# Kernel tuning notes

Hardware: AMD Instinct MI355X
Metric: run time of the kernel (lower is better)

## Reference

```python
import jax, jax.numpy as jnp
import numpy as np

T, NA, ND, E, H, L = 4, 20000, 20000, 100000, 128, 2


def setup_inputs() -> dict:
    key = jax.random.key(0)
    ks = jax.random.split(key, 16)
    f = lambda k, s: jax.random.normal(k, s, dtype=jnp.float32)
    s = 0.05  # weight init scale
    inp = {
        "x_a": f(ks[0], (T, NA, H)),
        "x_d": f(ks[1], (T, ND, H)),
        "ea_ad": f(ks[2], (T, E, H)),
        "ea_da": f(ks[3], (T, E, H)),
        # edge_index rows: [src, dst]
        "ei_ad": jax.random.randint(ks[4], (T, 2, E), 0, NA, dtype=jnp.int32),
        "ei_da": jax.random.randint(ks[5], (T, 2, E), 0, ND, dtype=jnp.int32),
    }
    i = 6
    for et in ("ad", "da"):
        inp[f"w1_{et}"] = f(ks[i], (T, L, H, H)) * s; i += 1
        inp[f"b1_{et}"] = jnp.zeros((T, L, H), jnp.float32)
        inp[f"w2_{et}"] = f(ks[i], (T, L, H, H)) * s; i += 1
        inp[f"b2_{et}"] = jnp.zeros((T, L, H), jnp.float32)
        inp[f"eps_{et}"] = jnp.zeros((T, L), jnp.float32)
    return inp


def _gine(x_src, x_dst, ei, ea, w1, b1, w2, b2, eps, n_dst):
    # GINEConv: MLP((1+eps)*x_dst + sum_j relu(x_src[j] + edge_attr))
    msg = jax.nn.relu(x_src[ei[0]] + ea)                      # (E, H)
    agg = jax.ops.segment_sum(msg, ei[1], num_segments=n_dst)  # (n_dst, H)
    h = (1.0 + eps) * x_dst + agg
    return jax.nn.relu(h @ w1 + b1) @ w2 + b2


def _one_timestep(xa, xd, ea_ad, ea_da, ei_ad, ei_da,
                  w1_ad, b1_ad, w2_ad, b2_ad, eps_ad,
                  w1_da, b1_da, w2_da, b2_da, eps_da):
    for l in range(L):
        # hetero layer: both edge-type convs read the same layer input
        xd_new = _gine(xa, xd, ei_ad, ea_ad, w1_ad[l], b1_ad[l], w2_ad[l], b2_ad[l], eps_ad[l], ND)
        xa_new = _gine(xd, xa, ei_da, ea_da, w1_da[l], b1_da[l], w2_da[l], b2_da[l], eps_da[l], NA)
        xa, xd = xa_new, xd_new
        if l < L - 1:
            xa, xd = jax.nn.relu(xa), jax.nn.relu(xd)
    return xa, xd


def reference(x_a, x_d, ea_ad, ea_da, ei_ad, ei_da,
              w1_ad, b1_ad, w2_ad, b2_ad, eps_ad,
              w1_da, b1_da, w2_da, b2_da, eps_da):
    # one independent hetero-GNN per timestep (ModuleList) -> vmap over T
    xa_out, xd_out = jax.vmap(_one_timestep)(
        x_a, x_d, ea_ad, ea_da, ei_ad, ei_da,
        w1_ad, b1_ad, w2_ad, b2_ad, eps_ad,
        w1_da, b1_da, w2_da, b2_da, eps_da)
    return jnp.concatenate([xa_out, xd_out], axis=1)  # (T, NA+ND, H)
```

## Files before the change

### kernel.cpp

```cpp
#include <hip/hip_runtime.h>

#define KT 4
#define KN 20000
#define KE 100000
#define KH 128
#define KL 2
#define KNT 40000

typedef __attribute__((ext_vector_type(8))) short short8v;
typedef __attribute__((ext_vector_type(4))) float f32x4;

__device__ __forceinline__ short bf16rn(float x) {
    unsigned u = __float_as_uint(x);
    u = (u + 0x7fffu + ((u >> 16) & 1u)) >> 16;
    return (short)u;
}
__device__ __forceinline__ float bf16tof(short h) {
    return __uint_as_float(((unsigned)(unsigned short)h) << 16);
}
__device__ __forceinline__ short8v mk8(uint2 a, uint2 b) {
    union { unsigned u[4]; short8v s; } c;
    c.u[0] = a.x; c.u[1] = a.y; c.u[2] = b.x; c.u[3] = b.y;
    return c.s;
}

__global__ void count_k(const int* __restrict__ ei_ad, const int* __restrict__ ei_da,
                        int* __restrict__ cnt) {
    int e = blockIdx.x * 256 + threadIdx.x;
    int z = blockIdx.y;
    if (e >= KE) return;
    int t = z >> 1, et = z & 1;
    const int* ei = et ? ei_da : ei_ad;
    int dst = ei[(t * 2 + 1) * KE + e];
    atomicAdd(&cnt[z * KN + dst], 1);
}

__global__ void scan_k(int* __restrict__ cnt, int* __restrict__ offs) {
    __shared__ int s[256];
    int z = blockIdx.x, tid = threadIdx.x;
    const int CH = (KN + 255) / 256;
    int n0 = tid * CH;
    int lim = n0 < KN ? min(CH, KN - n0) : 0;
    long base = (long)z * KN + n0;
    int sum = 0;
    for (int i = 0; i < lim; ++i) sum += cnt[base + i];
    s[tid] = sum;
    __syncthreads();
    for (int off = 1; off < 256; off <<= 1) {
        int v = (tid >= off) ? s[tid - off] : 0;
        __syncthreads();
        s[tid] += v;
        __syncthreads();
    }
    int run = s[tid] - sum;
    for (int i = 0; i < lim; ++i) {
        int c = cnt[base + i];
        offs[(long)z * (KN + 1) + n0 + i] = run;
        cnt[base + i] = run;
        run += c;
    }
    if (tid == 0) offs[(long)z * (KN + 1) + KN] = KE;
}

__global__ void fill_k(const int* __restrict__ ei_ad, const int* __restrict__ ei_da,
                       int* __restrict__ cur, int2* __restrict__ pes) {
    int e = blockIdx.x * 256 + threadIdx.x;
    int z = blockIdx.y;
    if (e >= KE) return;
    int t = z >> 1, et = z & 1;
    const int* ei = et ? ei_da : ei_ad;
    int src = ei[(t * 2 + 0) * KE + e];
    int dst = ei[(t * 2 + 1) * KE + e];
    int pos = atomicAdd(&cur[z * KN + dst], 1);
    pes[(long)z * KE + pos] = make_int2(e, src);
}

__global__ __launch_bounds__(256)
void agg_k(const float* __restrict__ xa_base, long xa_ts,
           const float* __restrict__ xd_base, long xd_ts,
           const float* __restrict__ ea_ad, const float* __restrict__ ea_da,
           const float* __restrict__ eps_ad, const float* __restrict__ eps_da,
           const int* __restrict__ offs, const int2* __restrict__ pes,
           short* __restrict__ agg_hi, short* __restrict__ agg_lo, int l) {
    int z = blockIdx.y, t = z >> 1, et = z & 1;
    int li = threadIdx.x & 31;
    int node = blockIdx.x * 8 + (threadIdx.x >> 5);

    const float* ea  = (et ? ea_da : ea_ad) + (long)t * KE * KH;
    const float* eps = et ? eps_da : eps_ad;
    const float* src = et ? (xd_base + t * xd_ts) : (xa_base + t * xa_ts);
    const float* dst = et ? (xa_base + t * xa_ts) : (xd_base + t * xd_ts);
    const int2*  pz  = pes + (long)z * KE;

    int beg = offs[(long)z * (KN + 1) + node];
    int end = offs[(long)z * (KN + 1) + node + 1];
    float scale = 1.0f + eps[t * KL + l];

    float4 dv = *(const float4*)(dst + (long)node * KH + li * 4);
    float4 acc = make_float4(0.f, 0.f, 0.f, 0.f);

    if (beg < end) {
        int last = end - 1;
        for (int i = beg; i < end; i += 4) {
            int i0 = min(i, last), i1 = min(i + 1, last),
                i2 = min(i + 2, last), i3 = min(i + 3, last);
            int2 p0 = pz[i0], p1 = pz[i1], p2 = pz[i2], p3 = pz[i3];
            float4 e0 = *(const float4*)(ea + (long)p0.x * KH + li * 4);
            float4 e1 = *(const float4*)(ea + (long)p1.x * KH + li * 4);
            float4 e2 = *(const float4*)(ea + (long)p2.x * KH + li * 4);
            float4 e3 = *(const float4*)(ea + (long)p3.x * KH + li * 4);
            float4 x0 = *(const float4*)(src + (long)p0.y * KH + li * 4);
            float4 x1 = *(const float4*)(src + (long)p1.y * KH + li * 4);
            float4 x2 = *(const float4*)(src + (long)p2.y * KH + li * 4);
            float4 x3 = *(const float4*)(src + (long)p3.y * KH + li * 4);
            float4 es4[4] = {e0, e1, e2, e3};
            float4 xs[4] = {x0, x1, x2, x3};
            #pragma unroll
            for (int u = 0; u < 4; ++u) {
                float m = (i + u <= last) ? 1.0f : 0.0f;
                acc.x = fmaf(m, fmaxf(xs[u].x + es4[u].x, 0.f), acc.x);
                acc.y = fmaf(m, fmaxf(xs[u].y + es4[u].y, 0.f), acc.y);
                acc.z = fmaf(m, fmaxf(xs[u].z + es4[u].z, 0.f), acc.z);
                acc.w = fmaf(m, fmaxf(xs[u].w + es4[u].w, 0.f), acc.w);
            }
        }
    }

    float4 r;
    r.x = fmaf(scale, dv.x, acc.x);
    r.y = fmaf(scale, dv.y, acc.y);
    r.z = fmaf(scale, dv.z, acc.z);
    r.w = fmaf(scale, dv.w, acc.w);

    unsigned short h0 = (unsigned short)bf16rn(r.x);
    unsigned short h1 = (unsigned short)bf16rn(r.y);
    unsigned short h2 = (unsigned short)bf16rn(r.z);
    unsigned short h3 = (unsigned short)bf16rn(r.w);
    unsigned short l0 = (unsigned short)bf16rn(r.x - bf16tof((short)h0));
    unsigned short l1 = (unsigned short)bf16rn(r.y - bf16tof((short)h1));
    unsigned short l2 = (unsigned short)bf16rn(r.z - bf16tof((short)h2));
    unsigned short l3 = (unsigned short)bf16rn(r.w - bf16tof((short)h3));
    long o = ((long)z * KN + node) * KH + li * 4;
    *(uint2*)(agg_hi + o) = make_uint2(((unsigned)h1 << 16) | h0, ((unsigned)h3 << 16) | h2);
    *(uint2*)(agg_lo + o) = make_uint2(((unsigned)l1 << 16) | l0, ((unsigned)l3 << 16) | l2);
}

__global__ __launch_bounds__(256)
void wsplit_k(const float* __restrict__ w1_ad, const float* __restrict__ w1_da,
              const float* __restrict__ w2_ad, const float* __restrict__ w2_da,
              short* __restrict__ wsp) {
    int mat = blockIdx.x >> 3, part = blockIdx.x & 7;
    int arr = mat >> 3, rem = mat & 7;
    const float* src = (arr == 0 ? w1_ad : arr == 1 ? w1_da : arr == 2 ? w2_ad : w2_da)
                       + (long)rem * KH * KH;
    #pragma unroll
    for (int p = 0; p < 8; ++p) {
        int idx = part * 2048 + p * 256 + threadIdx.x;
        int k = idx >> 7, c = idx & 127;
        float v = src[idx];
        short hi = bf16rn(v);
        short lo = bf16rn(v - bf16tof(hi));
        int chunk = k >> 5, kk = k & 31;
        long ohi = ((long)(mat * 2 + 0) * 4 + chunk) * 4096 + c * 32 + kk;
        long olo = ((long)(mat * 2 + 1) * 4 + chunk) * 4096 + c * 32 + kk;
        wsp[ohi] = hi;
        wsp[olo] = lo;
    }
}

__global__ __launch_bounds__(256)
void fused_k(const short* __restrict__ agg_hi, const short* __restrict__ agg_lo,
             const short* __restrict__ wsp,
             const float* __restrict__ b1_ad, const float* __restrict__ b1_da,
             const float* __restrict__ b2_ad, const float* __restrict__ b2_da,
             float* __restrict__ d_out, int l) {
    __shared__ short midh[128][132];
    __shared__ short midl[128][132];

    int z = blockIdx.y, t = z >> 1, et = z & 1;
    int tid = threadIdx.x;
    int mat1 = (0 * 2 + et) * 8 + t * 2 + l;
    int mat2 = (1 * 2 + et) * 8 + t * 2 + l;
    const float* Bp1 = (et ? b1_da : b1_ad) + (long)(t * KL + l) * KH;
    const float* Bp2 = (et ? b2_da : b2_ad) + (long)(t * KL + l) * KH;
    int r0 = blockIdx.x * 128;

    int lane = tid & 63, wid = tid >> 6;
    int wr = wid >> 1, wc = wid & 1;
    int lrow = lane & 15, lq = lane >> 4;

    f32x4 acc[4][4];
    #pragma unroll
    for (int i = 0; i < 4; ++i)
        #pragma unroll
        for (int j = 0; j < 4; ++j) acc[i][j] = (f32x4){0.f, 0.f, 0.f, 0.f};

    #pragma unroll
    for (int kc = 0; kc < 4; ++kc) {
        const short* whp = wsp + ((long)(mat1 * 2 + 0) * 4 + kc) * 4096;
        const short* wlp = wsp + ((long)(mat1 * 2 + 1) * 4 + kc) * 4096;
        short8v bhi[4], blo[4];
        #pragma unroll
        for (int j = 0; j < 4; ++j) {
            int off = (wc * 64 + j * 16 + lrow) * 32 + lq * 8;
            bhi[j] = *(const short8v*)(whp + off);
            blo[j] = *(const short8v*)(wlp + off);
        }
        #pragma unroll
        for (int i = 0; i < 4; ++i) {
            int row = min(r0 + wr * 64 + i * 16 + lrow, KN - 1);
            long o = ((long)z * KN + row) * KH + kc * 32 + lq * 8;
            short8v ahi = *(const short8v*)(agg_hi + o);
            short8v alo = *(const short8v*)(agg_lo + o);
            #pragma unroll
            for (int j = 0; j < 4; ++j) {
                acc[i][j] = __builtin_amdgcn_mfma_f32_16x16x32_bf16(bhi[j], ahi, acc[i][j], 0, 0, 0);
                acc[i][j] = __builtin_amdgcn_mfma_f32_16x16x32_bf16(blo[j], ahi, acc[i][j], 0, 0, 0);
                acc[i][j] = __builtin_amdgcn_mfma_f32_16x16x32_bf16(bhi[j], alo, acc[i][j], 0, 0, 0);
            }
        }
    }

    #pragma unroll
    for (int i = 0; i < 4; ++i) {
        int lr = wr * 64 + i * 16 + lrow;
        #pragma unroll
        for (int j = 0; j < 4; ++j) {
            int col = wc * 64 + j * 16 + lq * 4;
            float4 b4 = *(const float4*)&Bp1[col];
            f32x4 a = acc[i][j];
            float v0 = fmaxf(a[0] + b4.x, 0.f);
            float v1 = fmaxf(a[1] + b4.y, 0.f);
            float v2 = fmaxf(a[2] + b4.z, 0.f);
            float v3 = fmaxf(a[3] + b4.w, 0.f);
            unsigned short h0 = (unsigned short)bf16rn(v0);
            unsigned short h1 = (unsigned short)bf16rn(v1);
            unsigned short h2 = (unsigned short)bf16rn(v2);
            unsigned short h3 = (unsigned short)bf16rn(v3);
            unsigned short q0 = (unsigned short)bf16rn(v0 - bf16tof((short)h0));
            unsigned short q1 = (unsigned short)bf16rn(v1 - bf16tof((short)h1));
            unsigned short q2 = (unsigned short)bf16rn(v2 - bf16tof((short)h2));
            unsigned short q3 = (unsigned short)bf16rn(v3 - bf16tof((short)h3));
            *(uint2*)&midh[lr][col] = make_uint2(((unsigned)h1 << 16) | h0,
                                                 ((unsigned)h3 << 16) | h2);
            *(uint2*)&midl[lr][col] = make_uint2(((unsigned)q1 << 16) | q0,
                                                 ((unsigned)q3 << 16) | q2);
        }
    }
    __syncthreads();

    #pragma unroll
    for (int i = 0; i < 4; ++i)
        #pragma unroll
        for (int j = 0; j < 4; ++j) acc[i][j] = (f32x4){0.f, 0.f, 0.f, 0.f};

    #pragma unroll
    for (int kc = 0; kc < 4; ++kc) {
        const short* whp = wsp + ((long)(mat2 * 2 + 0) * 4 + kc) * 4096;
        const short* wlp = wsp + ((long)(mat2 * 2 + 1) * 4 + kc) * 4096;
        short8v bhi[4], blo[4];
        #pragma unroll
        for (int j = 0; j < 4; ++j) {
            int off = (wc * 64 + j * 16 + lrow) * 32 + lq * 8;
            bhi[j] = *(const short8v*)(whp + off);
            blo[j] = *(const short8v*)(wlp + off);
        }
        #pragma unroll
        for (int i = 0; i < 4; ++i) {
            int lr = wr * 64 + i * 16 + lrow;
            int co = kc * 32 + lq * 8;
            uint2 ha = *(const uint2*)&midh[lr][co];
            uint2 hb = *(const uint2*)&midh[lr][co + 4];
            uint2 la = *(const uint2*)&midl[lr][co];
            uint2 lb = *(const uint2*)&midl[lr][co + 4];
            short8v ahi = mk8(ha, hb);
            short8v alo = mk8(la, lb);
            #pragma unroll
            for (int j = 0; j < 4; ++j) {
                acc[i][j] = __builtin_amdgcn_mfma_f32_16x16x32_bf16(bhi[j], ahi, acc[i][j], 0, 0, 0);
                acc[i][j] = __builtin_amdgcn_mfma_f32_16x16x32_bf16(blo[j], ahi, acc[i][j], 0, 0, 0);
                acc[i][j] = __builtin_amdgcn_mfma_f32_16x16x32_bf16(bhi[j], alo, acc[i][j], 0, 0, 0);
            }
        }
    }

    int relu = (l == 0) ? 1 : 0;
    #pragma unroll
    for (int i = 0; i < 4; ++i) {
        int node = r0 + wr * 64 + i * 16 + lrow;
        if (node >= KN) continue;
        #pragma unroll
        for (int j = 0; j < 4; ++j) {
            int col = wc * 64 + j * 16 + lq * 4;
            float4 b4 = *(const float4*)&Bp2[col];
            f32x4 a = acc[i][j];
            float4 v;
            v.x = a[0] + b4.x; v.y = a[1] + b4.y;
            v.z = a[2] + b4.z; v.w = a[3] + b4.w;
            if (relu) {
                v.x = fmaxf(v.x, 0.f); v.y = fmaxf(v.y, 0.f);
                v.z = fmaxf(v.z, 0.f); v.w = fmaxf(v.w, 0.f);
            }
            long off = (long)t * KNT * KH + (et == 0 ? (long)KN * KH : 0)
                     + (long)node * KH + col;
            *(float4*)&d_out[off] = v;
        }
    }
}

extern "C" void kernel_launch(void* const* d_in, const int* in_sizes, int n_in,
                              void* d_out_v, int out_size, void* d_ws, size_t ws_size,
                              hipStream_t stream) {
    const float* x_a    = (const float*)d_in[0];
    const float* x_d    = (const float*)d_in[1];
    const float* ea_ad  = (const float*)d_in[2];
    const float* ea_da  = (const float*)d_in[3];
    const int*   ei_ad  = (const int*)d_in[4];
    const int*   ei_da  = (const int*)d_in[5];
    const float* w1_ad  = (const float*)d_in[6];
    const float* b1_ad  = (const float*)d_in[7];
    const float* w2_ad  = (const float*)d_in[8];
    const float* b2_ad  = (const float*)d_in[9];
    const float* eps_ad = (const float*)d_in[10];
    const float* w1_da  = (const float*)d_in[11];
    const float* b1_da  = (const float*)d_in[12];
    const float* w2_da  = (const float*)d_in[13];
    const float* b2_da  = (const float*)d_in[14];
    const float* eps_da = (const float*)d_in[15];
    float* out = (float*)d_out_v;

    size_t nEl = (size_t)8 * KN * KH;
    short* agg_hi = (short*)d_ws;
    short* agg_lo = agg_hi + nEl;
    int*   offs   = (int*)(agg_lo + nEl);
    int*   cur    = offs + (size_t)8 * (KN + 1);
    int2*  pes    = (int2*)(cur + (size_t)8 * KN);
    short* wsp    = (short*)(pes + (size_t)8 * KE);

    hipMemsetAsync(cur, 0, (size_t)8 * KN * sizeof(int), stream);
    wsplit_k<<<256, 256, 0, stream>>>(w1_ad, w1_da, w2_ad, w2_da, wsp);

    dim3 eg((KE + 255) / 256, 8);
    count_k<<<eg, 256, 0, stream>>>(ei_ad, ei_da, cur);
    scan_k<<<8, 256, 0, stream>>>(cur, offs);
    fill_k<<<eg, 256, 0, stream>>>(ei_ad, ei_da, cur, pes);

    dim3 ag(KN / 8, 8);
    dim3 gg((KN + 127) / 128, 8);

    for (int l = 0; l < KL; ++l) {
        const float* xab; long xats;
        const float* xdb; long xdts;
        if (l == 0) {
            xab = x_a; xats = (long)KN * KH;
            xdb = x_d; xdts = (long)KN * KH;
        } else {
            xab = out;                 xats = (long)KNT * KH;
            xdb = out + (long)KN * KH; xdts = (long)KNT * KH;
        }
        agg_k<<<ag, 256, 0, stream>>>(xab, xats, xdb, xdts,
                                      ea_ad, ea_da, eps_ad, eps_da,
                                      offs, pes, agg_hi, agg_lo, l);
        fused_k<<<gg, 256, 0, stream>>>(agg_hi, agg_lo, wsp,
                                        b1_ad, b1_da, b2_ad, b2_da, out, l);
    }
}
```

Measured before the change: 577.0 us.

## Drop low-half bf16 split for activations and launch per-timestep kernels

Activations (aggregated features and the hidden MLP output) are now stored only as a single bf16 value instead of a hi/lo split, which removes the third MFMA per tile, the lo buffer traffic and half the shared-memory tile. Weights still keep the hi/lo split. Separately, the layer loop now runs per timestep, launching agg_k and fused_k with grid y=2 for each t instead of covering all 8 (t, edge-type) pairs in one launch. This cuts memory traffic and matrix work but lowers activation precision to plain bf16. It also launches four times as many kernels, each with a smaller grid, which may lower occupancy on the many-CU device.

Result: slower. 591.0 us (+2.4%).

```diff
diff --git a/kernel.cpp b/kernel.cpp
--- a/kernel.cpp
+++ b/kernel.cpp
@@ -81,8 +81,8 @@
            const float* __restrict__ ea_ad, const float* __restrict__ ea_da,
            const float* __restrict__ eps_ad, const float* __restrict__ eps_da,
            const int* __restrict__ offs, const int2* __restrict__ pes,
-           short* __restrict__ agg_hi, short* __restrict__ agg_lo, int l) {
-    int z = blockIdx.y, t = z >> 1, et = z & 1;
+           short* __restrict__ agg_b, int t, int l) {
+    int et = blockIdx.y, z = t * 2 + et;
     int li = threadIdx.x & 31;
     int node = blockIdx.x * 8 + (threadIdx.x >> 5);
 
@@ -136,13 +136,9 @@
     unsigned short h1 = (unsigned short)bf16rn(r.y);
     unsigned short h2 = (unsigned short)bf16rn(r.z);
     unsigned short h3 = (unsigned short)bf16rn(r.w);
-    unsigned short l0 = (unsigned short)bf16rn(r.x - bf16tof((short)h0));
-    unsigned short l1 = (unsigned short)bf16rn(r.y - bf16tof((short)h1));
-    unsigned short l2 = (unsigned short)bf16rn(r.z - bf16tof((short)h2));
-    unsigned short l3 = (unsigned short)bf16rn(r.w - bf16tof((short)h3));
     long o = ((long)z * KN + node) * KH + li * 4;
-    *(uint2*)(agg_hi + o) = make_uint2(((unsigned)h1 << 16) | h0, ((unsigned)h3 << 16) | h2);
-    *(uint2*)(agg_lo + o) = make_uint2(((unsigned)l1 << 16) | l0, ((unsigned)l3 << 16) | l2);
+    *(uint2*)(agg_b + o) = make_uint2(((unsigned)h1 << 16) | h0,
+                                      ((unsigned)h3 << 16) | h2);
 }
 
 __global__ __launch_bounds__(256)
@@ -169,15 +165,14 @@
 }
 
 __global__ __launch_bounds__(256)
-void fused_k(const short* __restrict__ agg_hi, const short* __restrict__ agg_lo,
+void fused_k(const short* __restrict__ agg_b,
              const short* __restrict__ wsp,
              const float* __restrict__ b1_ad, const float* __restrict__ b1_da,
              const float* __restrict__ b2_ad, const float* __restrict__ b2_da,
-             float* __restrict__ d_out, int l) {
+             float* __restrict__ d_out, int t, int l) {
     __shared__ short midh[128][132];
-    __shared__ short midl[128][132];
-
-    int z = blockIdx.y, t = z >> 1, et = z & 1;
+
+    int et = blockIdx.y, z = t * 2 + et;
     int tid = threadIdx.x;
     int mat1 = (0 * 2 + et) * 8 + t * 2 + l;
     int mat2 = (1 * 2 + et) * 8 + t * 2 + l;
@@ -210,13 +205,11 @@
         for (int i = 0; i < 4; ++i) {
             int row = min(r0 + wr * 64 + i * 16 + lrow, KN - 1);
             long o = ((long)z * KN + row) * KH + kc * 32 + lq * 8;
-            short8v ahi = *(const short8v*)(agg_hi + o);
-            short8v alo = *(const short8v*)(agg_lo + o);
+            short8v ahi = *(const short8v*)(agg_b + o);
             #pragma unroll
             for (int j = 0; j < 4; ++j) {
                 acc[i][j] = __builtin_amdgcn_mfma_f32_16x16x32_bf16(bhi[j], ahi, acc[i][j], 0, 0, 0);
                 acc[i][j] = __builtin_amdgcn_mfma_f32_16x16x32_bf16(blo[j], ahi, acc[i][j], 0, 0, 0);
-                acc[i][j] = __builtin_amdgcn_mfma_f32_16x16x32_bf16(bhi[j], alo, acc[i][j], 0, 0, 0);
             }
         }
     }
@@ -237,14 +230,8 @@
             unsigned short h1 = (unsigned short)bf16rn(v1);
             unsigned short h2 = (unsigned short)bf16rn(v2);
             unsigned short h3 = (unsigned short)bf16rn(v3);
-            unsigned short q0 = (unsigned short)bf16rn(v0 - bf16tof((short)h0));
-            unsigned short q1 = (unsigned short)bf16rn(v1 - bf16tof((short)h1));
-            unsigned short q2 = (unsigned short)bf16rn(v2 - bf16tof((short)h2));
-            unsigned short q3 = (unsigned short)bf16rn(v3 - bf16tof((short)h3));
             *(uint2*)&midh[lr][col] = make_uint2(((unsigned)h1 << 16) | h0,
                                                  ((unsigned)h3 << 16) | h2);
-            *(uint2*)&midl[lr][col] = make_uint2(((unsigned)q1 << 16) | q0,
-                                                 ((unsigned)q3 << 16) | q2);
         }
     }
     __syncthreads();
@@ -271,15 +258,11 @@
             int co = kc * 32 + lq * 8;
             uint2 ha = *(const uint2*)&midh[lr][co];
             uint2 hb = *(const uint2*)&midh[lr][co + 4];
-            uint2 la = *(const uint2*)&midl[lr][co];
-            uint2 lb = *(const uint2*)&midl[lr][co + 4];
             short8v ahi = mk8(ha, hb);
-            short8v alo = mk8(la, lb);
             #pragma unroll
             for (int j = 0; j < 4; ++j) {
                 acc[i][j] = __builtin_amdgcn_mfma_f32_16x16x32_bf16(bhi[j], ahi, acc[i][j], 0, 0, 0);
                 acc[i][j] = __builtin_amdgcn_mfma_f32_16x16x32_bf16(blo[j], ahi, acc[i][j], 0, 0, 0);
-                acc[i][j] = __builtin_amdgcn_mfma_f32_16x16x32_bf16(bhi[j], alo, acc[i][j], 0, 0, 0);
             }
         }
     }
@@ -330,12 +313,11 @@
     float* out = (float*)d_out_v;
 
     size_t nEl = (size_t)8 * KN * KH;
-    short* agg_hi = (short*)d_ws;
-    short* agg_lo = agg_hi + nEl;
-    int*   offs   = (int*)(agg_lo + nEl);
-    int*   cur    = offs + (size_t)8 * (KN + 1);
-    int2*  pes    = (int2*)(cur + (size_t)8 * KN);
-    short* wsp    = (short*)(pes + (size_t)8 * KE);
+    short* agg_b = (short*)d_ws;
+    int*   offs  = (int*)(agg_b + nEl);
+    int*   cur   = offs + (size_t)8 * (KN + 1);
+    int2*  pes   = (int2*)(cur + (size_t)8 * KN);
+    short* wsp   = (short*)(pes + (size_t)8 * KE);
 
     hipMemsetAsync(cur, 0, (size_t)8 * KN * sizeof(int), stream);
     wsplit_k<<<256, 256, 0, stream>>>(w1_ad, w1_da, w2_ad, w2_da, wsp);
@@ -345,23 +327,26 @@
     scan_k<<<8, 256, 0, stream>>>(cur, offs);
     fill_k<<<eg, 256, 0, stream>>>(ei_ad, ei_da, cur, pes);
 
-    dim3 ag(KN / 8, 8);
-    dim3 gg((KN + 127) / 128, 8);
-
-    for (int l = 0; l < KL; ++l) {
-        const float* xab; long xats;
-        const float* xdb; long xdts;
-        if (l == 0) {
-            xab = x_a; xats = (long)KN * KH;
-            xdb = x_d; xdts = (long)KN * KH;
-        } else {
-            xab = out;                 xats = (long)KNT * KH;
-            xdb = out + (long)KN * KH; xdts = (long)KNT * KH;
-        }
-        agg_k<<<ag, 256, 0, stream>>>(xab, xats, xdb, xdts,
-                                      ea_ad, ea_da, eps_ad, eps_da,
-                                      offs, pes, agg_hi, agg_lo, l);
-        fused_k<<<gg, 256, 0, stream>>>(agg_hi, agg_lo, wsp,
-                                        b1_ad, b1_da, b2_ad, b2_da, out, l);
-    }
-}
+    dim3 ag(KN / 8, 2);
+    dim3 gg((KN + 127) / 128, 2);
+
+    for (int t = 0; t < KT; ++t) {
+        for (int l = 0; l < KL; ++l) {
+            const float* xab; long xats;
+            const float* xdb; long xdts;
+            if (l == 0) {
+                xab = x_a; xats = (long)KN * KH;
+                xdb = x_d; xdts = (long)KN * KH;
+            } else {
+                xab = out;                 xats = (long)KNT * KH;
+                xdb = out + (long)KN * KH; xdts = (long)KNT * KH;
+            }
+            agg_k<<<ag, 256, 0, stream>>>(xab, xats, xdb, xdts,
+                                          ea_ad, ea_da, eps_ad, eps_da,
+                                          offs, pes, agg_b, t, l);
+            fused_k<<<gg, 256, 0, stream>>>(agg_b, wsp,
+                                            b1_ad, b1_da, b2_ad, b2_da,
+                                            out, t, l);
+        }
+    }
+}
```
